# Optimization experiments

Hardware: AMD Instinct MI355X
Metric: run time of the kernel (lower is better)

The kernel has to match this reference:

```python
import jax, jax.numpy as jnp
import numpy as np

B, N = 8, 2048
D_IN, D_FEAT, H, K = 2, 30, 64, 8
D_ATT = D_IN + D_FEAT + H  # 96, per-head attention input dim
ALPHA = 0.2
NEG = -1e9


def setup_inputs() -> dict:
    key = jax.random.key(0)
    ks = jax.random.split(key, 11)
    inputs = jax.random.normal(ks[0], (B, N, D_IN), jnp.float32)
    envs_feat = jax.random.normal(ks[1], (B, N, D_FEAT), jnp.float32)
    state_t = jax.random.normal(ks[2], (B, N, H), jnp.float32)
    conn = jax.random.uniform(ks[3], (N, N)) < 0.05
    conn = conn | jnp.eye(N, dtype=bool)
    bias_mat = jnp.where(conn, 0.0, NEG).astype(jnp.float32)
    # xavier-ish init (gain 1.414)
    def xav(k, shape, fi, fo):
        lim = 1.414 * np.sqrt(6.0 / (fi + fo))
        return jax.random.uniform(k, shape, jnp.float32, -lim, lim)
    W_h = xav(ks[4], (K, D_ATT, H), D_ATT, H)      # stacked per-head W
    a1_h = xav(ks[5], (K, H), H, 1)
    a2_h = xav(ks[6], (K, H), H, 1)
    W_o = xav(ks[7], (K * H, H), K * H, H)
    a1_o = xav(ks[8], (H,), H, 1)
    a2_o = xav(ks[9], (H,), H, 1)
    return {"inputs": inputs, "envs_feat": envs_feat, "state_t": state_t,
            "bias_mat": bias_mat, "W_h": W_h, "a1_h": a1_h, "a2_h": a2_h,
            "W_o": W_o, "a1_o": a1_o, "a2_o": a2_o}


def _gat_multihead(h, bias, W, a1, a2):
    # h: [b,n,d], W: [k,d,h], a1/a2: [k,h], bias: [n,n]
    Wh = jnp.einsum('bnd,kdh->bknh', h, W)
    f1 = jnp.einsum('bknh,kh->bkn', Wh, a1)
    f2 = jnp.einsum('bknh,kh->bkn', Wh, a2)
    e = jax.nn.leaky_relu(f1[:, :, :, None] + f2[:, :, None, :], ALPHA) + bias  # [b,k,n,n]
    att = jax.nn.softmax(e, axis=-1)
    return jnp.einsum('bknm,bkmh->bknh', att, Wh)  # [b,k,n,h]


def _gat_single(h, bias, W, a1, a2):
    # h: [b,n,d], W: [d,h], a1/a2: [h]
    Wh = jnp.einsum('bnd,dh->bnh', h, W)
    f1 = Wh @ a1  # [b,n]
    f2 = Wh @ a2
    e = jax.nn.leaky_relu(f1[:, :, None] + f2[:, None, :], ALPHA) + bias  # [b,n,n]
    att = jax.nn.softmax(e, axis=-1)
    return jnp.einsum('bnm,bmh->bnh', att, Wh)


def reference(inputs, envs_feat, state_t, bias_mat, W_h, a1_h, a2_h, W_o, a1_o, a2_o):
    b, n = inputs.shape[0], inputs.shape[1]
    h = jnp.concatenate([inputs, envs_feat, state_t], axis=2)  # [b,n,D_ATT]
    hp = _gat_multihead(h, bias_mat, W_h, a1_h, a2_h)          # [b,k,n,h]
    h1 = jax.nn.elu(hp)
    h1 = jnp.transpose(h1, (0, 2, 1, 3)).reshape(b, n, -1)     # concat heads: [b,n,k*h]
    out = jax.nn.elu(_gat_single(h1, bias_mat, W_o, a1_o, a2_o))
    return out
```

## Files before the change

kernel.cpp:

```cpp
#include <hip/hip_runtime.h>
#include <hip/hip_bf16.h>
#include <math.h>

#define B   8
#define N   2048
#define DIN 2
#define DF  30
#define HH  64
#define KK  8
#define DATT 96
#define CAP 384
#define CAPL 176
#define ALPHA 0.2f

__device__ __forceinline__ float lrelu(float x) { return x > 0.f ? x : ALPHA * x; }
__device__ __forceinline__ float elu1(float x)  { return x > 0.f ? x : (__expf(x) - 1.f); }
__device__ __forceinline__ unsigned short f2bf(float x) {
    __hip_bfloat16 h = __float2bfloat16(x);
    return *reinterpret_cast<unsigned short*>(&h);
}
__device__ __forceinline__ float dot2bf(unsigned a, unsigned b, float acc) {
    asm("v_dot2_f32_bf16 %0, %1, %2, %0" : "+v"(acc) : "v"(a), "v"(b));
    return acc;
}

__global__ void k_mask(const float* __restrict__ bias, int* __restrict__ cols,
                       int* __restrict__ cnt) {
    int i = blockIdx.x * 4 + (threadIdx.x >> 6);
    int lane = threadIdx.x & 63;
    int c = 0;
    for (int j0 = 0; j0 < N; j0 += 64) {
        float v = bias[(size_t)i * N + j0 + lane];
        bool conn = v > -1e8f;
        unsigned long long m = __ballot(conn);
        if (conn) {
            int pos = c + __popcll(m & ((1ull << lane) - 1ull));
            if (pos < CAP) cols[i * CAP + pos] = j0 + lane;
        }
        c += __popcll(m);
    }
    if (lane == 0) cnt[i] = c < CAP ? c : CAP;
}

__global__ void k_wh(const float* __restrict__ inp, const float* __restrict__ envs,
                     const float* __restrict__ st,  const float* __restrict__ W_h,
                     const float* __restrict__ a1,  const float* __restrict__ a2,
                     unsigned short* __restrict__ Whb,
                     float* __restrict__ f1n, float* __restrict__ f2n) {
    __shared__ float hs[32 * 100];
    int k = blockIdx.y, b = blockIdx.z;
    int i0 = blockIdx.x * 32;
    int tid = threadIdx.x, lane = tid & 63, w = tid >> 6;

#pragma unroll
    for (int rep = 0; rep < 2; ++rep) {
        int idx = rep * 256 + tid;
        int row = idx >> 4, q = idx & 15;
        float4 v = *(const float4*)&st[(size_t)(b * N + i0 + row) * HH + q * 4];
        float* hb = &hs[row * 100 + DIN + DF + q * 4];
        hb[0] = v.x; hb[1] = v.y; hb[2] = v.z; hb[3] = v.w;
    }
#pragma unroll
    for (int rep = 0; rep < 2; ++rep) {
        int idx = rep * 256 + tid;
        if (idx < 480) {
            int row = idx / 15, q = idx % 15;
            float2 v = *(const float2*)&envs[(size_t)(b * N + i0 + row) * DF + q * 2];
            float* hb = &hs[row * 100 + DIN + q * 2];
            hb[0] = v.x; hb[1] = v.y;
        }
    }
    if (tid < 64) {
        int row = tid >> 1, q = tid & 1;
        hs[row * 100 + q] = inp[(size_t)(b * N + i0 + row) * DIN + q];
    }

    const float* Wk = W_h + (size_t)k * DATT * HH + lane;
    float Wv[DATT];
#pragma unroll
    for (int d = 0; d < DATT; ++d) Wv[d] = Wk[(size_t)d * HH];
    float a1k = a1[k * HH + lane], a2k = a2[k * HH + lane];

    __syncthreads();

    for (int rr = 0; rr < 8; ++rr) {
        int r = w * 8 + rr;
        const float* hb = &hs[r * 100];
        float acc0 = 0.f, acc1 = 0.f;
#pragma unroll
        for (int d = 0; d < DATT; d += 2) {
            float2 hv = *(const float2*)&hb[d];
            acc0 += hv.x * Wv[d];
            acc1 += hv.y * Wv[d + 1];
        }
        float acc = acc0 + acc1;
        int i = i0 + r;
        Whb[((size_t)(b * N + i)) * (KK * HH) + k * HH + lane] = f2bf(acc);
        float p1 = acc * a1k, p2 = acc * a2k;
#pragma unroll
        for (int off = 32; off; off >>= 1) {
            p1 += __shfl_xor(p1, off);
            p2 += __shfl_xor(p2, off);
        }
        if (lane == 0) {
            f1n[((size_t)(b * N + i)) * KK + k] = p1;
            f2n[((size_t)(b * N + i)) * KK + k] = p2;
        }
    }
}

__global__ void k_attn(const unsigned short* __restrict__ Whb, const float* __restrict__ f1n,
                       const float* __restrict__ f2n, const int* __restrict__ cols,
                       const int* __restrict__ cnt, unsigned short* __restrict__ h1b) {
    __shared__ unsigned short swb[4][8][200];
    __shared__ int jl[4][CAPL];
    int flat = blockIdx.y * (N / 4) + blockIdx.x;
    int b = flat & 7, tile = flat >> 3;
    int tid = threadIdx.x, lane = tid & 63, w = tid >> 6;
    int i = tile * 4 + w;
    int k = lane >> 3, q = lane & 7;

    int c = cnt[i]; if (c > CAPL) c = CAPL;
    const int* cl = cols + (size_t)i * CAP;
    for (int e = lane; e < c; e += 64) jl[w][e] = cl[e];
    if (lane == 0 && (c & 1)) jl[w][c] = 0;

    float f1k = f1n[((size_t)(b * N + i)) * KK + k];
    const float* f2b = f2n + (size_t)b * N * KK;

    float s[22];
    float mk = -1e30f;
#pragma unroll
    for (int t = 0; t < 22; ++t) {
        int e = t * 8 + q;
        int ee = e < c ? e : c - 1;
        int j = jl[w][ee];
        float sc = lrelu(f1k + f2b[j * KK + k]);
        if (e >= c) sc = -1e30f;
        s[t] = sc;
        mk = fmaxf(mk, sc);
    }
#pragma unroll
    for (int off = 4; off; off >>= 1) mk = fmaxf(mk, __shfl_xor(mk, off));

    float Zk = 0.f;
#pragma unroll
    for (int t = 0; t < 22; ++t) {
        float wt = __expf(s[t] - mk);
        Zk += wt;
        swb[w][k][t * 8 + q] = f2bf(wt);
    }
#pragma unroll
    for (int off = 4; off; off >>= 1) Zk += __shfl_xor(Zk, off);
    float invZ = 1.f / Zk;

    const char* Wp = (const char*)Whb + (size_t)b * N * 1024;
    float a0 = 0.f, a1_ = 0.f, a2_ = 0.f, a3_ = 0.f;
    float a4 = 0.f, a5 = 0.f, a6 = 0.f, a7 = 0.f;
    int lane16 = lane << 4;
    int cpad = (c + 1) & ~1;
#pragma unroll 4
    for (int e0 = 0; e0 < cpad; e0 += 2) {
        int j0 = __builtin_amdgcn_readfirstlane(jl[w][e0]);
        int j1 = __builtin_amdgcn_readfirstlane(jl[w][e0 + 1]);
        unsigned wp = *(const unsigned*)&swb[w][k][e0];
        uint4 v0 = *(const uint4*)(Wp + ((size_t)j0 << 10) + lane16);
        uint4 v1 = *(const uint4*)(Wp + ((size_t)j1 << 10) + lane16);
        a0 = dot2bf(__builtin_amdgcn_perm(v1.x, v0.x, 0x05040100u), wp, a0);
        a1_ = dot2bf(__builtin_amdgcn_perm(v1.x, v0.x, 0x07060302u), wp, a1_);
        a2_ = dot2bf(__builtin_amdgcn_perm(v1.y, v0.y, 0x05040100u), wp, a2_);
        a3_ = dot2bf(__builtin_amdgcn_perm(v1.y, v0.y, 0x07060302u), wp, a3_);
        a4 = dot2bf(__builtin_amdgcn_perm(v1.z, v0.z, 0x05040100u), wp, a4);
        a5 = dot2bf(__builtin_amdgcn_perm(v1.z, v0.z, 0x07060302u), wp, a5);
        a6 = dot2bf(__builtin_amdgcn_perm(v1.w, v0.w, 0x05040100u), wp, a6);
        a7 = dot2bf(__builtin_amdgcn_perm(v1.w, v0.w, 0x07060302u), wp, a7);
    }
    uint4 ov;
    ov.x = (unsigned)f2bf(elu1(a0 * invZ)) | ((unsigned)f2bf(elu1(a1_ * invZ)) << 16);
    ov.y = (unsigned)f2bf(elu1(a2_ * invZ)) | ((unsigned)f2bf(elu1(a3_ * invZ)) << 16);
    ov.z = (unsigned)f2bf(elu1(a4 * invZ)) | ((unsigned)f2bf(elu1(a5 * invZ)) << 16);
    ov.w = (unsigned)f2bf(elu1(a6 * invZ)) | ((unsigned)f2bf(elu1(a7 * invZ)) << 16);
    *(uint4*)&h1b[((size_t)(b * N + i)) * (KK * HH) + lane * 8] = ov;
}

__global__ void k_who(const unsigned short* __restrict__ h1b, const float* __restrict__ W_o,
                      const float* __restrict__ a1o, const float* __restrict__ a2o,
                      float* __restrict__ Who, float* __restrict__ f1o,
                      float* __restrict__ f2o) {
    __shared__ unsigned Wsp[64][64];
    int tid = threadIdx.x, lane = tid & 63, w = tid >> 6;
    int g = lane >> 4, sub = lane & 15;
    int row = blockIdx.x * 16 + w * 4 + g;
    const unsigned short* hp = h1b + (size_t)row * (KK * HH);
    float ax = 0.f, ay = 0.f, az = 0.f, aw = 0.f;
    for (int ph = 0; ph < 4; ++ph) {
        __syncthreads();
#pragma unroll
        for (int rep = 0; rep < 16; ++rep) {
            int idx = rep * 256 + tid;
            int t = idx >> 6, h = idx & 63;
            const float* wp = W_o + (size_t)(ph * 128 + 2 * t) * HH + h;
            Wsp[t][h] = (unsigned)f2bf(wp[0]) | ((unsigned)f2bf(wp[HH]) << 16);
        }
        __syncthreads();
        uint4 hv = *(const uint4*)&hp[ph * 128 + sub * 8];
#pragma unroll
        for (int t = 0; t < 64; ++t) {
            unsigned src = (t & 3) == 0 ? hv.x : (t & 3) == 1 ? hv.y
                         : (t & 3) == 2 ? hv.z : hv.w;
            unsigned hpair = (unsigned)__shfl((int)src, t >> 2, 16);
            uint4 wv = *(const uint4*)&Wsp[t][sub * 4];
            ax = dot2bf(hpair, wv.x, ax);
            ay = dot2bf(hpair, wv.y, ay);
            az = dot2bf(hpair, wv.z, az);
            aw = dot2bf(hpair, wv.w, aw);
        }
    }
    float4 acc = make_float4(ax, ay, az, aw);
    *(float4*)&Who[(size_t)row * HH + sub * 4] = acc;
    float4 a1v = *(const float4*)&a1o[sub * 4];
    float4 a2v = *(const float4*)&a2o[sub * 4];
    float p1 = acc.x * a1v.x + acc.y * a1v.y + acc.z * a1v.z + acc.w * a1v.w;
    float p2 = acc.x * a2v.x + acc.y * a2v.y + acc.z * a2v.z + acc.w * a2v.w;
#pragma unroll
    for (int off = 8; off; off >>= 1) {
        p1 += __shfl_xor(p1, off);
        p2 += __shfl_xor(p2, off);
    }
    if (sub == 0) { f1o[row] = p1; f2o[row] = p2; }
}

__global__ void k_attn2(const float* __restrict__ Who, const float* __restrict__ f1o,
                        const float* __restrict__ f2o, const int* __restrict__ cols,
                        const int* __restrict__ cnt, float* __restrict__ out) {
    __shared__ float2 sedge[16][CAPL + 2];
    int flat = blockIdx.y * 128 + blockIdx.x;
    int b = flat & 7;
    int tile = flat >> 3;
    int tid = threadIdx.x;
    int lane = tid & 63, w = tid >> 6;
    int g = lane >> 4, sub = lane & 15;
    int r = w * 4 + g;
    int i = tile * 16 + r;

    int c = cnt[i]; if (c > CAPL) c = CAPL;
    float f1i = f1o[b * N + i];
    const int* cl = cols + (size_t)i * CAP;
    const float* f2p = f2o + (size_t)b * N;

    float m = -1e30f;
    for (int e = sub; e < c; e += 16) {
        int j = cl[e];
        float sc = lrelu(f1i + f2p[j]);
        sedge[r][e] = make_float2(__int_as_float(j << 8), sc);
        m = fmaxf(m, sc);
    }
#pragma unroll
    for (int off = 8; off; off >>= 1) m = fmaxf(m, __shfl_xor(m, off));

    float Z = 0.f;
    for (int e = sub; e < c; e += 16) {
        float wt = __expf(sedge[r][e].y - m);
        sedge[r][e].y = wt;
        Z += wt;
    }
#pragma unroll
    for (int off = 8; off; off >>= 1) Z += __shfl_xor(Z, off);
    float invZ = 1.f / Z;

    const char* Wp = (const char*)(Who + (size_t)b * N * HH);
    int lane4 = sub << 4;
    float4 acc = make_float4(0.f, 0.f, 0.f, 0.f);
    int e = 0;
    for (; e + 4 <= c; e += 4) {
        float2 p0 = sedge[r][e];
        float2 p1 = sedge[r][e + 1];
        float2 p2 = sedge[r][e + 2];
        float2 p3 = sedge[r][e + 3];
        float4 v0 = *(const float4*)(Wp + (__float_as_int(p0.x) + lane4));
        float4 v1 = *(const float4*)(Wp + (__float_as_int(p1.x) + lane4));
        float4 v2 = *(const float4*)(Wp + (__float_as_int(p2.x) + lane4));
        float4 v3 = *(const float4*)(Wp + (__float_as_int(p3.x) + lane4));
        acc.x += p0.y * v0.x; acc.y += p0.y * v0.y;
        acc.z += p0.y * v0.z; acc.w += p0.y * v0.w;
        acc.x += p1.y * v1.x; acc.y += p1.y * v1.y;
        acc.z += p1.y * v1.z; acc.w += p1.y * v1.w;
        acc.x += p2.y * v2.x; acc.y += p2.y * v2.y;
        acc.z += p2.y * v2.z; acc.w += p2.y * v2.w;
        acc.x += p3.y * v3.x; acc.y += p3.y * v3.y;
        acc.z += p3.y * v3.z; acc.w += p3.y * v3.w;
    }
    for (; e < c; ++e) {
        float2 p0 = sedge[r][e];
        float4 v0 = *(const float4*)(Wp + (__float_as_int(p0.x) + lane4));
        acc.x += p0.y * v0.x; acc.y += p0.y * v0.y;
        acc.z += p0.y * v0.z; acc.w += p0.y * v0.w;
    }
    float4 o;
    o.x = elu1(acc.x * invZ); o.y = elu1(acc.y * invZ);
    o.z = elu1(acc.z * invZ); o.w = elu1(acc.w * invZ);
    *(float4*)&out[(size_t)(b * N + i) * HH + sub * 4] = o;
}

extern "C" void kernel_launch(void* const* d_in, const int* in_sizes, int n_in,
                              void* d_out, int out_size, void* d_ws, size_t ws_size,
                              hipStream_t stream) {
    const float* inp   = (const float*)d_in[0];
    const float* envs  = (const float*)d_in[1];
    const float* st    = (const float*)d_in[2];
    const float* bias  = (const float*)d_in[3];
    const float* W_h   = (const float*)d_in[4];
    const float* a1_h  = (const float*)d_in[5];
    const float* a2_h  = (const float*)d_in[6];
    const float* W_o   = (const float*)d_in[7];
    const float* a1_o  = (const float*)d_in[8];
    const float* a2_o  = (const float*)d_in[9];
    float* out = (float*)d_out;

    char* ws = (char*)d_ws;
    size_t off = 0;
    unsigned short* Whb = (unsigned short*)(ws + off); off += (size_t)B * N * KK * HH * 2;
    unsigned short* h1b = (unsigned short*)(ws + off); off += (size_t)B * N * KK * HH * 2;
    float* f1n = (float*)(ws + off); off += (size_t)B * N * KK * 4;
    float* f2n = (float*)(ws + off); off += (size_t)B * N * KK * 4;
    float* Who = (float*)(ws + off); off += (size_t)B * N * HH * 4;
    float* f1o = (float*)(ws + off); off += (size_t)B * N * 4;
    float* f2o = (float*)(ws + off); off += (size_t)B * N * 4;
    int*   cols = (int*)(ws + off);  off += (size_t)N * CAP * 4;
    int*   cnt  = (int*)(ws + off);  off += (size_t)N * 4;

    k_mask<<<dim3(N / 4), dim3(256), 0, stream>>>(bias, cols, cnt);
    k_wh<<<dim3(N / 32, KK, B), dim3(256), 0, stream>>>(inp, envs, st, W_h, a1_h, a2_h,
                                                        Whb, f1n, f2n);
    k_attn<<<dim3(N / 4, B), dim3(256), 0, stream>>>(Whb, f1n, f2n, cols, cnt, h1b);
    k_who<<<dim3(B * N / 16), dim3(256), 0, stream>>>(h1b, W_o, a1_o, a2_o, Who, f1o, f2o);
    k_attn2<<<dim3(N / 16, B), dim3(256), 0, stream>>>(Who, f1o, f2o, cols, cnt, out);
}
```

Baseline: 268.0 us.

## Merge mask and Wh kernels; store second-layer Wh in bf16 with dot2 gather

Fuses the mask-compaction kernel and the per-head projection kernel into one launch by splitting the block range, which removes one launch and lets the two independent jobs overlap. The output-layer projection Who is now stored in bf16 instead of fp32, halving the bytes gathered per neighbour in the second attention pass. That pass keeps scores in registers with a fixed 11-iteration unrolled loop, stores the weights as bf16 and accumulates edge pairs with v_dot2 bf16 instructions. Rounding Who and the attention weights to bf16 lowers precision, and the unrolled loop assumes at most 176 neighbours per row.

```diff
diff --git a/kernel.cpp b/kernel.cpp
--- a/kernel.cpp
+++ b/kernel.cpp
@@ -24,33 +24,36 @@
     return acc;
 }
 
-__global__ void k_mask(const float* __restrict__ bias, int* __restrict__ cols,
-                       int* __restrict__ cnt) {
-    int i = blockIdx.x * 4 + (threadIdx.x >> 6);
-    int lane = threadIdx.x & 63;
-    int c = 0;
-    for (int j0 = 0; j0 < N; j0 += 64) {
-        float v = bias[(size_t)i * N + j0 + lane];
-        bool conn = v > -1e8f;
-        unsigned long long m = __ballot(conn);
-        if (conn) {
-            int pos = c + __popcll(m & ((1ull << lane) - 1ull));
-            if (pos < CAP) cols[i * CAP + pos] = j0 + lane;
-        }
-        c += __popcll(m);
-    }
-    if (lane == 0) cnt[i] = c < CAP ? c : CAP;
-}
-
-__global__ void k_wh(const float* __restrict__ inp, const float* __restrict__ envs,
-                     const float* __restrict__ st,  const float* __restrict__ W_h,
-                     const float* __restrict__ a1,  const float* __restrict__ a2,
-                     unsigned short* __restrict__ Whb,
-                     float* __restrict__ f1n, float* __restrict__ f2n) {
+__global__ void k_prep(const float* __restrict__ bias, int* __restrict__ cols,
+                       int* __restrict__ cnt,
+                       const float* __restrict__ inp, const float* __restrict__ envs,
+                       const float* __restrict__ st,  const float* __restrict__ W_h,
+                       const float* __restrict__ a1,  const float* __restrict__ a2,
+                       unsigned short* __restrict__ Whb,
+                       float* __restrict__ f1n, float* __restrict__ f2n) {
     __shared__ float hs[32 * 100];
-    int k = blockIdx.y, b = blockIdx.z;
-    int i0 = blockIdx.x * 32;
     int tid = threadIdx.x, lane = tid & 63, w = tid >> 6;
+
+    if (blockIdx.x < 512) {
+        int i = blockIdx.x * 4 + w;
+        int c = 0;
+        for (int j0 = 0; j0 < N; j0 += 64) {
+            float v = bias[(size_t)i * N + j0 + lane];
+            bool conn = v > -1e8f;
+            unsigned long long m = __ballot(conn);
+            if (conn) {
+                int pos = c + __popcll(m & ((1ull << lane) - 1ull));
+                if (pos < CAP) cols[i * CAP + pos] = j0 + lane;
+            }
+            c += __popcll(m);
+        }
+        if (lane == 0) cnt[i] = c < CAP ? c : CAP;
+        return;
+    }
+
+    int x = blockIdx.x - 512;
+    int tile = x & 63, k = (x >> 6) & 7, b = x >> 9;
+    int i0 = tile * 32;
 
 #pragma unroll
     for (int rep = 0; rep < 2; ++rep) {
@@ -185,7 +188,7 @@
 
 __global__ void k_who(const unsigned short* __restrict__ h1b, const float* __restrict__ W_o,
                       const float* __restrict__ a1o, const float* __restrict__ a2o,
-                      float* __restrict__ Who, float* __restrict__ f1o,
+                      unsigned short* __restrict__ Whob, float* __restrict__ f1o,
                       float* __restrict__ f2o) {
     __shared__ unsigned Wsp[64][64];
     int tid = threadIdx.x, lane = tid & 63, w = tid >> 6;
@@ -216,12 +219,13 @@
             aw = dot2bf(hpair, wv.w, aw);
         }
     }
-    float4 acc = make_float4(ax, ay, az, aw);
-    *(float4*)&Who[(size_t)row * HH + sub * 4] = acc;
+    unsigned lo = (unsigned)f2bf(ax) | ((unsigned)f2bf(ay) << 16);
+    unsigned hi = (unsigned)f2bf(az) | ((unsigned)f2bf(aw) << 16);
+    *(uint2*)&Whob[(size_t)row * HH + sub * 4] = make_uint2(lo, hi);
     float4 a1v = *(const float4*)&a1o[sub * 4];
     float4 a2v = *(const float4*)&a2o[sub * 4];
-    float p1 = acc.x * a1v.x + acc.y * a1v.y + acc.z * a1v.z + acc.w * a1v.w;
-    float p2 = acc.x * a2v.x + acc.y * a2v.y + acc.z * a2v.z + acc.w * a2v.w;
+    float p1 = ax * a1v.x + ay * a1v.y + az * a1v.z + aw * a1v.w;
+    float p2 = ax * a2v.x + ay * a2v.y + az * a2v.z + aw * a2v.w;
 #pragma unroll
     for (int off = 8; off; off >>= 1) {
         p1 += __shfl_xor(p1, off);
@@ -230,10 +234,11 @@
     if (sub == 0) { f1o[row] = p1; f2o[row] = p2; }
 }
 
-__global__ void k_attn2(const float* __restrict__ Who, const float* __restrict__ f1o,
+__global__ void k_attn2(const unsigned short* __restrict__ Whob, const float* __restrict__ f1o,
                         const float* __restrict__ f2o, const int* __restrict__ cols,
                         const int* __restrict__ cnt, float* __restrict__ out) {
-    __shared__ float2 sedge[16][CAPL + 2];
+    __shared__ int            jo[16][184];
+    __shared__ unsigned short swb2[16][184];
     int flat = blockIdx.y * 128 + blockIdx.x;
     int b = flat & 7;
     int tile = flat >> 3;
@@ -248,57 +253,53 @@
     const int* cl = cols + (size_t)i * CAP;
     const float* f2p = f2o + (size_t)b * N;
 
+    float s2[11];
     float m = -1e30f;
-    for (int e = sub; e < c; e += 16) {
-        int j = cl[e];
+#pragma unroll
+    for (int t = 0; t < 11; ++t) {
+        int e = t * 16 + sub;
+        int ee = e < c ? e : c - 1;
+        int j = cl[ee];
+        if (e < c) jo[r][e] = j << 7;
         float sc = lrelu(f1i + f2p[j]);
-        sedge[r][e] = make_float2(__int_as_float(j << 8), sc);
+        if (e >= c) sc = -1e30f;
+        s2[t] = sc;
         m = fmaxf(m, sc);
     }
 #pragma unroll
     for (int off = 8; off; off >>= 1) m = fmaxf(m, __shfl_xor(m, off));
 
     float Z = 0.f;
-    for (int e = sub; e < c; e += 16) {
-        float wt = __expf(sedge[r][e].y - m);
-        sedge[r][e].y = wt;
+#pragma unroll
+    for (int t = 0; t < 11; ++t) {
+        int e = t * 16 + sub;
+        float wt = __expf(s2[t] - m);
         Z += wt;
+        if (e < c) swb2[r][e] = f2bf(wt);
     }
 #pragma unroll
     for (int off = 8; off; off >>= 1) Z += __shfl_xor(Z, off);
     float invZ = 1.f / Z;
 
-    const char* Wp = (const char*)(Who + (size_t)b * N * HH);
-    int lane4 = sub << 4;
-    float4 acc = make_float4(0.f, 0.f, 0.f, 0.f);
-    int e = 0;
-    for (; e + 4 <= c; e += 4) {
-        float2 p0 = sedge[r][e];
-        float2 p1 = sedge[r][e + 1];
-        float2 p2 = sedge[r][e + 2];
-        float2 p3 = sedge[r][e + 3];
-        float4 v0 = *(const float4*)(Wp + (__float_as_int(p0.x) + lane4));
-        float4 v1 = *(const float4*)(Wp + (__float_as_int(p1.x) + lane4));
-        float4 v2 = *(const float4*)(Wp + (__float_as_int(p2.x) + lane4));
-        float4 v3 = *(const float4*)(Wp + (__float_as_int(p3.x) + lane4));
-        acc.x += p0.y * v0.x; acc.y += p0.y * v0.y;
-        acc.z += p0.y * v0.z; acc.w += p0.y * v0.w;
-        acc.x += p1.y * v1.x; acc.y += p1.y * v1.y;
-        acc.z += p1.y * v1.z; acc.w += p1.y * v1.w;
-        acc.x += p2.y * v2.x; acc.y += p2.y * v2.y;
-        acc.z += p2.y * v2.z; acc.w += p2.y * v2.w;
-        acc.x += p3.y * v3.x; acc.y += p3.y * v3.y;
-        acc.z += p3.y * v3.z; acc.w += p3.y * v3.w;
-    }
-    for (; e < c; ++e) {
-        float2 p0 = sedge[r][e];
-        float4 v0 = *(const float4*)(Wp + (__float_as_int(p0.x) + lane4));
-        acc.x += p0.y * v0.x; acc.y += p0.y * v0.y;
-        acc.z += p0.y * v0.z; acc.w += p0.y * v0.w;
+    if (sub == 0 && (c & 1)) { jo[r][c] = 0; swb2[r][c] = 0; }
+
+    const char* Wp = (const char*)Whob + (size_t)b * N * 128;
+    float a0 = 0.f, a1_ = 0.f, a2_ = 0.f, a3_ = 0.f;
+    int lane8 = sub << 3;
+    int cpad = (c + 1) & ~1;
+    for (int e0 = 0; e0 < cpad; e0 += 2) {
+        int2 jp = *(const int2*)&jo[r][e0];
+        unsigned wp = *(const unsigned*)&swb2[r][e0];
+        uint2 v0 = *(const uint2*)(Wp + jp.x + lane8);
+        uint2 v1 = *(const uint2*)(Wp + jp.y + lane8);
+        a0 = dot2bf(__builtin_amdgcn_perm(v1.x, v0.x, 0x05040100u), wp, a0);
+        a1_ = dot2bf(__builtin_amdgcn_perm(v1.x, v0.x, 0x07060302u), wp, a1_);
+        a2_ = dot2bf(__builtin_amdgcn_perm(v1.y, v0.y, 0x05040100u), wp, a2_);
+        a3_ = dot2bf(__builtin_amdgcn_perm(v1.y, v0.y, 0x07060302u), wp, a3_);
     }
     float4 o;
-    o.x = elu1(acc.x * invZ); o.y = elu1(acc.y * invZ);
-    o.z = elu1(acc.z * invZ); o.w = elu1(acc.w * invZ);
+    o.x = elu1(a0 * invZ); o.y = elu1(a1_ * invZ);
+    o.z = elu1(a2_ * invZ); o.w = elu1(a3_ * invZ);
     *(float4*)&out[(size_t)(b * N + i) * HH + sub * 4] = o;
 }
 
@@ -319,20 +320,20 @@
 
     char* ws = (char*)d_ws;
     size_t off = 0;
-    unsigned short* Whb = (unsigned short*)(ws + off); off += (size_t)B * N * KK * HH * 2;
-    unsigned short* h1b = (unsigned short*)(ws + off); off += (size_t)B * N * KK * HH * 2;
+    unsigned short* Whb  = (unsigned short*)(ws + off); off += (size_t)B * N * KK * HH * 2;
+    unsigned short* h1b  = (unsigned short*)(ws + off); off += (size_t)B * N * KK * HH * 2;
+    unsigned short* Whob = (unsigned short*)(ws + off); off += (size_t)B * N * HH * 2;
     float* f1n = (float*)(ws + off); off += (size_t)B * N * KK * 4;
     float* f2n = (float*)(ws + off); off += (size_t)B * N * KK * 4;
-    float* Who = (float*)(ws + off); off += (size_t)B * N * HH * 4;
     float* f1o = (float*)(ws + off); off += (size_t)B * N * 4;
     float* f2o = (float*)(ws + off); off += (size_t)B * N * 4;
     int*   cols = (int*)(ws + off);  off += (size_t)N * CAP * 4;
     int*   cnt  = (int*)(ws + off);  off += (size_t)N * 4;
 
-    k_mask<<<dim3(N / 4), dim3(256), 0, stream>>>(bias, cols, cnt);
-    k_wh<<<dim3(N / 32, KK, B), dim3(256), 0, stream>>>(inp, envs, st, W_h, a1_h, a2_h,
-                                                        Whb, f1n, f2n);
+    k_prep<<<dim3(512 + 4096), dim3(256), 0, stream>>>(bias, cols, cnt,
+                                                       inp, envs, st, W_h, a1_h, a2_h,
+                                                       Whb, f1n, f2n);
     k_attn<<<dim3(N / 4, B), dim3(256), 0, stream>>>(Whb, f1n, f2n, cols, cnt, h1b);
-    k_who<<<dim3(B * N / 16), dim3(256), 0, stream>>>(h1b, W_o, a1_o, a2_o, Who, f1o, f2o);
-    k_attn2<<<dim3(N / 16, B), dim3(256), 0, stream>>>(Who, f1o, f2o, cols, cnt, out);
-}
+    k_who<<<dim3(B * N / 16), dim3(256), 0, stream>>>(h1b, W_o, a1_o, a2_o, Whob, f1o, f2o);
+    k_attn2<<<dim3(N / 16, B), dim3(256), 0, stream>>>(Whob, f1o, f2o, cols, cnt, out);
+}
```

New measurement: 262.1 us. 1.02x faster.
